# Kernel optimization log

Measured on AMD Instinct MI355X. Metric: run time of the kernel, lower is better.

## Reference

```python
import jax, jax.numpy as jnp
import numpy as np

N = 100000
E = 1600000
NUM_GRAPHS = 64
EPS = 1e-5


def setup_inputs() -> dict:
    key = jax.random.key(0)
    ks = jax.random.split(key, 8)
    x = jax.random.normal(ks[0], (N, 128), dtype=jnp.float32)
    edge_index = jax.random.randint(ks[1], (2, E), 0, N, dtype=jnp.int64)
    batch = jnp.sort(jax.random.randint(ks[2], (N,), 0, NUM_GRAPHS, dtype=jnp.int64))
    W1 = jax.random.normal(ks[3], (128, 128), dtype=jnp.float32) * (1.0 / np.sqrt(128))
    W2 = jax.random.normal(ks[4], (128, 128), dtype=jnp.float32) * (1.0 / np.sqrt(128))
    W3 = jax.random.normal(ks[5], (128, 32), dtype=jnp.float32) * (1.0 / np.sqrt(128))
    return {
        'x': x, 'edge_index': edge_index, 'batch': batch,
        'W1': W1, 'b1': jnp.zeros((128,), jnp.float32),
        'W2': W2, 'b2': jnp.zeros((128,), jnp.float32),
        'W3': W3, 'b3': jnp.zeros((32,), jnp.float32),
        'gamma1': jnp.ones((128,), jnp.float32), 'beta1': jnp.zeros((128,), jnp.float32),
        'gamma2': jnp.ones((128,), jnp.float32), 'beta2': jnp.zeros((128,), jnp.float32),
    }


def _gcn_norm(edge_index, n_nodes):
    # PyG GCNConv default: add self-loops, symmetric normalization.
    loop = jnp.arange(n_nodes, dtype=edge_index.dtype)
    src = jnp.concatenate([edge_index[0], loop])  # [E+N]
    dst = jnp.concatenate([edge_index[1], loop])
    deg = jax.ops.segment_sum(jnp.ones_like(dst, dtype=jnp.float32), dst,
                              num_segments=n_nodes)
    dinv = jnp.where(deg > 0, jax.lax.rsqrt(deg), 0.0)
    norm = dinv[src] * dinv[dst]  # [E+N]
    return src, dst, norm


def _gcn_conv(x, W, b, src, dst, norm, n_nodes):
    h = x @ W                                   # [N, d_out] dense GEMM
    msg = h[src] * norm[:, None]                # gather + scale  [E+N, d_out]
    out = jax.ops.segment_sum(msg, dst, num_segments=n_nodes)  # scatter-add
    return out + b


def _batchnorm(x, gamma, beta):
    # Training-mode BatchNorm1d: batch stats over node dim, biased variance.
    mean = jnp.mean(x, axis=0)
    var = jnp.var(x, axis=0)
    return (x - mean) * jax.lax.rsqrt(var + EPS) * gamma + beta


def reference(x, edge_index, batch, W1, b1, W2, b2, W3, b3,
              gamma1, beta1, gamma2, beta2):
    src, dst, norm = _gcn_norm(edge_index, N)
    h = _gcn_conv(x, W1, b1, src, dst, norm, N)
    h = jax.nn.relu(_batchnorm(h, gamma1, beta1))  # dropout is identity (eval)
    h = _gcn_conv(h, W2, b2, src, dst, norm, N)
    h = jax.nn.relu(_batchnorm(h, gamma2, beta2))
    h = _gcn_conv(h, W3, b3, src, dst, norm, N)
    # global_mean_pool over graph ids
    sums = jax.ops.segment_sum(h, batch, num_segments=NUM_GRAPHS)  # [G, out]
    cnts = jax.ops.segment_sum(jnp.ones((N,), jnp.float32), batch,
                               num_segments=NUM_GRAPHS)
    pooled = sums / jnp.maximum(cnts, 1.0)[:, None]
    return jax.nn.sigmoid(pooled)
```

## Files before the change

### kernel.cpp

```cpp
#include <hip/hip_runtime.h>
#include <math.h>

#define NGRAPH 64
#define EPS_BN 1e-5f
#define BN_BLOCKS 512

typedef unsigned int uint32;
typedef unsigned short ushort16;
typedef __attribute__((ext_vector_type(8))) short short8v;
typedef __attribute__((ext_vector_type(4))) float float4v;

__device__ __forceinline__ float bf2f(uint32 u16) {
    return __uint_as_float(u16 << 16);
}
__device__ __forceinline__ ushort16 f2bf(float f) {
    uint32 u = __float_as_uint(f);
    return (ushort16)((u + 0x7fffu + ((u >> 16) & 1u)) >> 16);
}
__device__ __forceinline__ uint32 pack2(float lo, float hi) {
    return (uint32)f2bf(lo) | ((uint32)f2bf(hi) << 16);
}

__global__ __launch_bounds__(256) void k_cnt(const int* __restrict__ dst, int* cnt, int ne) {
    int i = blockIdx.x * 256 + threadIdx.x;
    if (i < ne) atomicAdd(&cnt[dst[i]], 1);
}

__global__ __launch_bounds__(1024) void k_scan1(const int* __restrict__ cnt,
                                                int* __restrict__ rowstart,
                                                int* __restrict__ blocksum,
                                                float* __restrict__ dinv, int n) {
    __shared__ int sh[1024];
    const int tid = threadIdx.x;
    const int i = blockIdx.x * 1024 + tid;
    int v = (i < n) ? cnt[i] : 0;
    if (i < n) dinv[i] = rsqrtf((float)(v + 1));
    sh[tid] = v;
    __syncthreads();
    for (int off = 1; off < 1024; off <<= 1) {
        int t = (tid >= off) ? sh[tid - off] : 0;
        __syncthreads();
        sh[tid] += t;
        __syncthreads();
    }
    if (i < n) rowstart[i] = sh[tid] - v;
    if (tid == 1023) blocksum[blockIdx.x] = sh[1023];
}

__global__ __launch_bounds__(1024) void k_scan2(int* __restrict__ blocksum, int nb) {
    __shared__ int sh[1024];
    const int tid = threadIdx.x;
    int v = (tid < nb) ? blocksum[tid] : 0;
    sh[tid] = v;
    __syncthreads();
    for (int off = 1; off < 1024; off <<= 1) {
        int t = (tid >= off) ? sh[tid - off] : 0;
        __syncthreads();
        sh[tid] += t;
        __syncthreads();
    }
    if (tid < nb) blocksum[tid] = sh[tid] - v;
}

__global__ __launch_bounds__(256) void k_scan3(int* __restrict__ rowstart,
                                               int* __restrict__ rowcur,
                                               const int* __restrict__ blocksum, int n) {
    int i = blockIdx.x * 256 + threadIdx.x;
    if (i < n) {
        int v = rowstart[i] + blocksum[i >> 10];
        rowstart[i] = v;
        rowcur[i] = v;
    }
}

#define SC_EPB 8
__global__ __launch_bounds__(256) void k_scatter_w(const int* __restrict__ src,
                                                   const int* __restrict__ dst,
                                                   int* __restrict__ rowcur,
                                                   int* __restrict__ esrc,
                                                   int ne, int wsz) {
    const int w = blockIdx.x & 7;
    const int chunk = blockIdx.x >> 3;
    const int wlo = w * wsz;
    const int whi = wlo + wsz;
    int base = chunk * (256 * SC_EPB) + threadIdx.x;
    #pragma unroll
    for (int j = 0; j < SC_EPB; ++j) {
        int i = base + j * 256;
        if (i < ne) {
            int d = dst[i];
            if (d >= wlo && d < whi) {
                int pos = atomicAdd(&rowcur[d], 1);
                esrc[pos] = src[i];
            }
        }
    }
}

__global__ __launch_bounds__(256) void k_wprep(const float* __restrict__ W,
                                               ushort16* __restrict__ Wt,
                                               int rows, int cols) {
    int i = blockIdx.x * 256 + threadIdx.x;
    if (i >= rows * cols) return;
    int c = i / rows, k = i % rows;
    Wt[i] = f2bf(W[k * cols + c]);
}

template<int COLS, bool BN, bool AF32>
__global__ __launch_bounds__(256) void k_gemm_mfma(const void* __restrict__ Av,
                                                   const ushort16* __restrict__ Wt,
                                                   const float* __restrict__ ss,
                                                   ushort16* __restrict__ C, int nrows) {
    constexpr int K = 128;
    constexpr int LDK = K + 8;
    __shared__ ushort16 As[64 * LDK];
    __shared__ ushort16 Bs[COLS * LDK];
    const int tid = threadIdx.x;
    const int row0 = blockIdx.x * 64;

    {
        const uint4* wg = (const uint4*)Wt;
        for (int i = tid; i < COLS * (K / 8); i += 256) {
            int r = i >> 4, c8 = i & 15;
            *(uint4*)&Bs[r * LDK + c8 * 8] = wg[i];
        }
    }
    if constexpr (AF32) {
        const float* A = (const float*)Av;
        for (int i = tid; i < 64 * (K / 4); i += 256) {
            int r = i >> 5, c4 = i & 31;
            float4 a;
            if (row0 + r < nrows) a = *(const float4*)&A[(size_t)(row0 + r) * K + c4 * 4];
            else a = make_float4(0.f, 0.f, 0.f, 0.f);
            if (BN) {
                float4 sc = *(const float4*)&ss[c4 * 4];
                float4 sh = *(const float4*)&ss[128 + c4 * 4];
                a.x = fmaxf(fmaf(a.x, sc.x, sh.x), 0.f);
                a.y = fmaxf(fmaf(a.y, sc.y, sh.y), 0.f);
                a.z = fmaxf(fmaf(a.z, sc.z, sh.z), 0.f);
                a.w = fmaxf(fmaf(a.w, sc.w, sh.w), 0.f);
            }
            ushort4 o;
            o.x = f2bf(a.x); o.y = f2bf(a.y); o.z = f2bf(a.z); o.w = f2bf(a.w);
            *(ushort4*)&As[r * LDK + c4 * 4] = o;
        }
    } else {
        const uint4* Ag = (const uint4*)Av;
        for (int i = tid; i < 64 * (K / 8); i += 256) {
            int r = i >> 4, c8 = i & 15;
            uint4 u;
            if (row0 + r < nrows) u = Ag[(size_t)(row0 + r) * 16 + c8];
            else u = make_uint4(0, 0, 0, 0);
            if (BN) {
                uint32 wv[4] = {u.x, u.y, u.z, u.w};
                #pragma unroll
                for (int t = 0; t < 4; ++t) {
                    int f = c8 * 8 + t * 2;
                    float lo = fmaxf(fmaf(bf2f(wv[t] & 0xffffu), ss[f],     ss[128 + f]),     0.f);
                    float hi = fmaxf(fmaf(bf2f(wv[t] >> 16),     ss[f + 1], ss[128 + f + 1]), 0.f);
                    wv[t] = pack2(lo, hi);
                }
                u.x = wv[0]; u.y = wv[1]; u.z = wv[2]; u.w = wv[3];
            }
            *(uint4*)&As[r * LDK + c8 * 8] = u;
        }
    }
    __syncthreads();

    const int w = tid >> 6;
    const int l = tid & 63;
    const int lr = l & 15;
    const int lg = l >> 4;
    constexpr int CT = COLS / 16;

    float4v acc[CT] = {};
    short8v afrag[4];
    #pragma unroll
    for (int kk = 0; kk < 4; ++kk)
        afrag[kk] = *(const short8v*)&As[(w * 16 + lr) * LDK + kk * 32 + lg * 8];
    #pragma unroll
    for (int kk = 0; kk < 4; ++kk) {
        #pragma unroll
        for (int ct = 0; ct < CT; ++ct) {
            short8v b = *(const short8v*)&Bs[(ct * 16 + lr) * LDK + kk * 32 + lg * 8];
            acc[ct] = __builtin_amdgcn_mfma_f32_16x16x32_bf16(afrag[kk], b, acc[ct], 0, 0, 0);
        }
    }
    #pragma unroll
    for (int ct = 0; ct < CT; ++ct) {
        #pragma unroll
        for (int r = 0; r < 4; ++r) {
            int gr = row0 + w * 16 + lg * 4 + r;
            if (gr < nrows) C[(size_t)gr * COLS + ct * 16 + lr] = f2bf(acc[ct][r]);
        }
    }
}

template<int COLS>
__global__ __launch_bounds__(256) void k_agg_csr(const ushort16* __restrict__ h,
                                                 const int* __restrict__ rowstart,
                                                 const int* __restrict__ cnt,
                                                 const int* __restrict__ esrc,
                                                 const float* __restrict__ dinv,
                                                 uint32* __restrict__ out, int n) {
    constexpr int TPN = COLS / 2;
    const uint32* __restrict__ hu = (const uint32*)h;
    int gt = blockIdx.x * 256 + threadIdx.x;
    int node = gt / TPN;
    if (node >= n) return;
    int lane = gt % TPN;

    float di = dinv[node];
    uint32 p = hu[(size_t)node * TPN + lane];
    float ax = bf2f(p & 0xffffu) * di * di;
    float ay = bf2f(p >> 16) * di * di;

    const int beg = rowstart[node];
    const int end = beg + cnt[node];
    int e = beg;
    for (; e + 4 <= end; e += 4) {
        int s0 = esrc[e], s1 = esrc[e + 1], s2 = esrc[e + 2], s3 = esrc[e + 3];
        float w0 = dinv[s0] * di, w1 = dinv[s1] * di;
        float w2 = dinv[s2] * di, w3 = dinv[s3] * di;
        uint32 p0 = hu[(size_t)s0 * TPN + lane];
        uint32 p1 = hu[(size_t)s1 * TPN + lane];
        uint32 p2 = hu[(size_t)s2 * TPN + lane];
        uint32 p3 = hu[(size_t)s3 * TPN + lane];
        ax = fmaf(bf2f(p0 & 0xffffu), w0, ax); ay = fmaf(bf2f(p0 >> 16), w0, ay);
        ax = fmaf(bf2f(p1 & 0xffffu), w1, ax); ay = fmaf(bf2f(p1 >> 16), w1, ay);
        ax = fmaf(bf2f(p2 & 0xffffu), w2, ax); ay = fmaf(bf2f(p2 >> 16), w2, ay);
        ax = fmaf(bf2f(p3 & 0xffffu), w3, ax); ay = fmaf(bf2f(p3 >> 16), w3, ay);
    }
    for (; e < end; ++e) {
        int s0 = esrc[e];
        float w0 = dinv[s0] * di;
        uint32 p0 = hu[(size_t)s0 * TPN + lane];
        ax = fmaf(bf2f(p0 & 0xffffu), w0, ax);
        ay = fmaf(bf2f(p0 >> 16), w0, ay);
    }
    out[(size_t)node * TPN + lane] = pack2(ax, ay);
}

__global__ __launch_bounds__(256) void k_bn_stats1(const uint32* __restrict__ x,
                                                   float* __restrict__ partials, int n) {
    const int cp = threadIdx.x & 63;
    const int rl = threadIdx.x >> 6;
    float s0 = 0.f, s1 = 0.f, q0 = 0.f, q1 = 0.f;
    for (int r = blockIdx.x * 4 + rl; r < n; r += BN_BLOCKS * 4) {
        uint32 u = x[(size_t)r * 64 + cp];
        float lo = bf2f(u & 0xffffu), hi = bf2f(u >> 16);
        s0 += lo; s1 += hi;
        q0 = fmaf(lo, lo, q0); q1 = fmaf(hi, hi, q1);
    }
    __shared__ float shs[4 * 128];
    __shared__ float shq[4 * 128];
    shs[rl * 128 + 2 * cp] = s0; shs[rl * 128 + 2 * cp + 1] = s1;
    shq[rl * 128 + 2 * cp] = q0; shq[rl * 128 + 2 * cp + 1] = q1;
    __syncthreads();
    int f = threadIdx.x;
    if (f < 128) {
        float s = shs[f] + shs[128 + f] + shs[256 + f] + shs[384 + f];
        float q = shq[f] + shq[128 + f] + shq[256 + f] + shq[384 + f];
        partials[(size_t)blockIdx.x * 256 + f] = s;
        partials[(size_t)blockIdx.x * 256 + 128 + f] = q;
    }
}

__global__ __launch_bounds__(256) void k_bn_stats2(const float* __restrict__ partials,
                                                   float* __restrict__ stats) {
    int j = threadIdx.x;
    float acc = 0.f;
    int r0 = blockIdx.x * (BN_BLOCKS / 8);
    for (int r = 0; r < BN_BLOCKS / 8; ++r)
        acc += partials[(size_t)(r0 + r) * 256 + j];
    atomicAdd(&stats[j], acc);
}

__global__ __launch_bounds__(128) void k_bn_final(const float* __restrict__ stats,
                                                  const float* __restrict__ gamma,
                                                  const float* __restrict__ beta,
                                                  float* __restrict__ ss, int n) {
    int f = threadIdx.x;
    float inv_n = 1.0f / (float)n;
    float mean = stats[f] * inv_n;
    float var = stats[128 + f] * inv_n - mean * mean;
    float scale = gamma[f] * rsqrtf(var + EPS_BN);
    ss[f] = scale;
    ss[128 + f] = beta[f] - mean * scale;
}

#define POOL_SLICE 128
__global__ __launch_bounds__(256) void k_pool2(const uint32* __restrict__ h3,
                                               const int* __restrict__ batch,
                                               float* __restrict__ sums,
                                               float* __restrict__ cnt, int n) {
    const int fp = threadIdx.x & 15;
    const int sub = threadIdx.x >> 4;
    int node0 = blockIdx.x * (16 * POOL_SLICE) + sub * POOL_SLICE;
    if (node0 >= n) return;
    int node1 = min(node0 + POOL_SLICE, n);

    int cur_g = batch[node0];
    float a0 = 0.f, a1 = 0.f, c = 0.f;
    for (int i = node0; i < node1; ++i) {
        int g = batch[i];
        if (g != cur_g) {
            atomicAdd(&sums[cur_g * 32 + 2 * fp], a0);
            atomicAdd(&sums[cur_g * 32 + 2 * fp + 1], a1);
            if (fp == 0) atomicAdd(&cnt[cur_g], c);
            a0 = 0.f; a1 = 0.f; c = 0.f; cur_g = g;
        }
        uint32 u = h3[(size_t)i * 16 + fp];
        a0 += bf2f(u & 0xffffu);
        a1 += bf2f(u >> 16);
        c += 1.f;
    }
    atomicAdd(&sums[cur_g * 32 + 2 * fp], a0);
    atomicAdd(&sums[cur_g * 32 + 2 * fp + 1], a1);
    if (fp == 0) atomicAdd(&cnt[cur_g], c);
}

__global__ __launch_bounds__(256) void k_final(const float* __restrict__ sums,
                                               const float* __restrict__ cnt,
                                               const float* __restrict__ b3,
                                               float* __restrict__ out) {
    int i = blockIdx.x * 256 + threadIdx.x;
    if (i >= NGRAPH * 32) return;
    int g = i >> 5;
    int f = i & 31;
    float c = fmaxf(cnt[g], 1.0f);
    float v = sums[i] / c + b3[f];
    out[i] = 1.0f / (1.0f + expf(-v));
}

extern "C" void kernel_launch(void* const* d_in, const int* in_sizes, int n_in,
                              void* d_out, int out_size, void* d_ws, size_t ws_size,
                              hipStream_t stream) {
    const float* x      = (const float*)d_in[0];
    const int*   eidx   = (const int*)d_in[1];
    const int*   batch  = (const int*)d_in[2];
    const float* W1     = (const float*)d_in[3];
    const float* W2     = (const float*)d_in[5];
    const float* W3     = (const float*)d_in[7];
    const float* b3     = (const float*)d_in[8];
    const float* gamma1 = (const float*)d_in[9];
    const float* beta1  = (const float*)d_in[10];
    const float* gamma2 = (const float*)d_in[11];
    const float* beta2  = (const float*)d_in[12];

    const int N = in_sizes[0] / 128;
    const int E = in_sizes[1] / 2;
    const int* src = eidx;
    const int* dst = eidx + E;

    size_t off = 0;
    auto carve = [&](size_t bytes) {
        char* p = (char*)d_ws + off;
        off += (bytes + 511) & ~(size_t)511;
        return p;
    };
    const size_t NB = (size_t)N * 128 * sizeof(float);
    ushort16* bufA  = (ushort16*)carve(NB / 2);
    uint32* bufB    = (uint32*)carve(NB / 2);
    int*   cnt      = (int*)carve((size_t)N * 4);
    int*   rowstart = (int*)carve((size_t)N * 4);
    int*   rowcur   = (int*)carve((size_t)N * 4);
    float* dinv     = (float*)carve((size_t)N * 4);
    int*   esrc     = (int*)carve((size_t)E * 4);
    ushort16* wt1   = (ushort16*)carve(128 * 128 * 2);
    ushort16* wt2   = (ushort16*)carve(128 * 128 * 2);
    ushort16* wt3   = (ushort16*)carve(32 * 128 * 2);
    float* stats    = (float*)carve(256 * 4);
    float* ss1      = (float*)carve(256 * 4);
    float* ss2      = (float*)carve(256 * 4);
    float* partials = (float*)carve((size_t)BN_BLOCKS * 256 * 4);
    int*   blocksum = (int*)carve(1024 * 4);
    float* psum     = (float*)carve(NGRAPH * 32 * 4);
    float* pcnt     = (float*)carve(NGRAPH * 4);
    (void)ws_size; (void)n_in; (void)out_size;

    const int nblkN   = (N + 255) / 256;
    const int nblkE   = (E + 255) / 256;
    const int nbScan  = (N + 1023) / 1024;
    const int nbGemm  = (N + 63) / 64;
    const int nblkAgg128 = ((size_t)N * 64 + 255) / 256;
    const int nblkAgg32  = ((size_t)N * 16 + 255) / 256;
    const int nblkPool   = (N + 16 * POOL_SLICE - 1) / (16 * POOL_SLICE);
    const int wsz        = (N + 7) / 8;
    const int nbScat     = ((E + 256 * SC_EPB - 1) / (256 * SC_EPB)) * 8;

    k_wprep<<<(128 * 128 + 255) / 256, 256, 0, stream>>>(W1, wt1, 128, 128);
    k_wprep<<<(128 * 128 + 255) / 256, 256, 0, stream>>>(W2, wt2, 128, 128);
    k_wprep<<<(32 * 128 + 255) / 256, 256, 0, stream>>>(W3, wt3, 128, 32);

    hipMemsetAsync(cnt, 0, (size_t)N * 4, stream);
    k_cnt<<<nblkE, 256, 0, stream>>>(dst, cnt, E);
    k_scan1<<<nbScan, 1024, 0, stream>>>(cnt, rowstart, blocksum, dinv, N);
    k_scan2<<<1, 1024, 0, stream>>>(blocksum, nbScan);
    k_scan3<<<nblkN, 256, 0, stream>>>(rowstart, rowcur, blocksum, N);
    k_scatter_w<<<nbScat, 256, 0, stream>>>(src, dst, rowcur, esrc, E, wsz);

    k_gemm_mfma<128, false, true><<<nbGemm, 256, 0, stream>>>(x, wt1, nullptr, bufA, N);
    k_agg_csr<128><<<nblkAgg128, 256, 0, stream>>>(bufA, rowstart, cnt, esrc, dinv, bufB, N);
    k_bn_stats1<<<BN_BLOCKS, 256, 0, stream>>>(bufB, partials, N);
    hipMemsetAsync(stats, 0, 256 * 4, stream);
    k_bn_stats2<<<8, 256, 0, stream>>>(partials, stats);
    k_bn_final<<<1, 128, 0, stream>>>(stats, gamma1, beta1, ss1, N);

    k_gemm_mfma<128, true, false><<<nbGemm, 256, 0, stream>>>(bufB, wt2, ss1, bufA, N);
    k_agg_csr<128><<<nblkAgg128, 256, 0, stream>>>(bufA, rowstart, cnt, esrc, dinv, bufB, N);
    k_bn_stats1<<<BN_BLOCKS, 256, 0, stream>>>(bufB, partials, N);
    hipMemsetAsync(stats, 0, 256 * 4, stream);
    k_bn_stats2<<<8, 256, 0, stream>>>(partials, stats);
    k_bn_final<<<1, 128, 0, stream>>>(stats, gamma2, beta2, ss2, N);

    k_gemm_mfma<32, true, false><<<nbGemm, 256, 0, stream>>>(bufB, wt3, ss2, bufA, N);
    k_agg_csr<32><<<nblkAgg32, 256, 0, stream>>>(bufA, rowstart, cnt, esrc, dinv, bufB, N);

    hipMemsetAsync(psum, 0, NGRAPH * 32 * 4, stream);
    hipMemsetAsync(pcnt, 0, NGRAPH * 4, stream);
    k_pool2<<<nblkPool, 256, 0, stream>>>(bufB, batch, psum, pcnt, N);
    k_final<<<(NGRAPH * 32 + 255) / 256, 256, 0, stream>>>(psum, pcnt, b3, (float*)d_out);
}
```

Measured before the change: 477.0 us.

## Window degree counting, merge weight prep, process two row tiles per GEMM block, unroll gather

The degree-count kernel now uses the same 8-way destination windowing as the scatter kernel, which keeps each block's atomics within a narrower address range. The three weight-prep launches are merged into a single kernel. The GEMM now computes two 64-row tiles per block, reusing the weight tile already staged in shared memory. The CSR aggregation loop is unrolled to 8 edges with all loads issued before the FMAs, to raise memory-level parallelism. The costs are that the count kernel rereads dst 8 times and the GEMM grid is halved.

```diff
diff --git a/kernel.cpp b/kernel.cpp
--- a/kernel.cpp
+++ b/kernel.cpp
@@ -21,9 +21,22 @@
     return (uint32)f2bf(lo) | ((uint32)f2bf(hi) << 16);
 }
 
-__global__ __launch_bounds__(256) void k_cnt(const int* __restrict__ dst, int* cnt, int ne) {
-    int i = blockIdx.x * 256 + threadIdx.x;
-    if (i < ne) atomicAdd(&cnt[dst[i]], 1);
+#define SC_EPB 8
+__global__ __launch_bounds__(256) void k_cnt_w(const int* __restrict__ dst, int* __restrict__ cnt,
+                                               int ne, int wsz) {
+    const int w = blockIdx.x & 7;
+    const int chunk = blockIdx.x >> 3;
+    const int wlo = w * wsz;
+    const int whi = wlo + wsz;
+    int base = chunk * (256 * SC_EPB) + threadIdx.x;
+    #pragma unroll
+    for (int j = 0; j < SC_EPB; ++j) {
+        int i = base + j * 256;
+        if (i < ne) {
+            int d = dst[i];
+            if (d >= wlo && d < whi) atomicAdd(&cnt[d], 1);
+        }
+    }
 }
 
 __global__ __launch_bounds__(1024) void k_scan1(const int* __restrict__ cnt,
@@ -73,7 +86,6 @@
     }
 }
 
-#define SC_EPB 8
 __global__ __launch_bounds__(256) void k_scatter_w(const int* __restrict__ src,
                                                    const int* __restrict__ dst,
                                                    int* __restrict__ rowcur,
@@ -97,13 +109,25 @@
     }
 }
 
-__global__ __launch_bounds__(256) void k_wprep(const float* __restrict__ W,
-                                               ushort16* __restrict__ Wt,
-                                               int rows, int cols) {
+__global__ __launch_bounds__(256) void k_wprep_all(const float* __restrict__ W1,
+                                                   const float* __restrict__ W2,
+                                                   const float* __restrict__ W3,
+                                                   ushort16* __restrict__ wt1,
+                                                   ushort16* __restrict__ wt2,
+                                                   ushort16* __restrict__ wt3) {
     int i = blockIdx.x * 256 + threadIdx.x;
-    if (i >= rows * cols) return;
-    int c = i / rows, k = i % rows;
-    Wt[i] = f2bf(W[k * cols + c]);
+    if (i < 16384) {
+        int c = i >> 7, k = i & 127;
+        wt1[i] = f2bf(W1[k * 128 + c]);
+    } else if (i < 32768) {
+        int j = i - 16384;
+        int c = j >> 7, k = j & 127;
+        wt2[j] = f2bf(W2[k * 128 + c]);
+    } else if (i < 36864) {
+        int j = i - 32768;
+        int c = j >> 7, k = j & 127;
+        wt3[j] = f2bf(W3[k * 32 + c]);
+    }
 }
 
 template<int COLS, bool BN, bool AF32>
@@ -116,7 +140,6 @@
     __shared__ ushort16 As[64 * LDK];
     __shared__ ushort16 Bs[COLS * LDK];
     const int tid = threadIdx.x;
-    const int row0 = blockIdx.x * 64;
 
     {
         const uint4* wg = (const uint4*)Wt;
@@ -125,47 +148,6 @@
             *(uint4*)&Bs[r * LDK + c8 * 8] = wg[i];
         }
     }
-    if constexpr (AF32) {
-        const float* A = (const float*)Av;
-        for (int i = tid; i < 64 * (K / 4); i += 256) {
-            int r = i >> 5, c4 = i & 31;
-            float4 a;
-            if (row0 + r < nrows) a = *(const float4*)&A[(size_t)(row0 + r) * K + c4 * 4];
-            else a = make_float4(0.f, 0.f, 0.f, 0.f);
-            if (BN) {
-                float4 sc = *(const float4*)&ss[c4 * 4];
-                float4 sh = *(const float4*)&ss[128 + c4 * 4];
-                a.x = fmaxf(fmaf(a.x, sc.x, sh.x), 0.f);
-                a.y = fmaxf(fmaf(a.y, sc.y, sh.y), 0.f);
-                a.z = fmaxf(fmaf(a.z, sc.z, sh.z), 0.f);
-                a.w = fmaxf(fmaf(a.w, sc.w, sh.w), 0.f);
-            }
-            ushort4 o;
-            o.x = f2bf(a.x); o.y = f2bf(a.y); o.z = f2bf(a.z); o.w = f2bf(a.w);
-            *(ushort4*)&As[r * LDK + c4 * 4] = o;
-        }
-    } else {
-        const uint4* Ag = (const uint4*)Av;
-        for (int i = tid; i < 64 * (K / 8); i += 256) {
-            int r = i >> 4, c8 = i & 15;
-            uint4 u;
-            if (row0 + r < nrows) u = Ag[(size_t)(row0 + r) * 16 + c8];
-            else u = make_uint4(0, 0, 0, 0);
-            if (BN) {
-                uint32 wv[4] = {u.x, u.y, u.z, u.w};
-                #pragma unroll
-                for (int t = 0; t < 4; ++t) {
-                    int f = c8 * 8 + t * 2;
-                    float lo = fmaxf(fmaf(bf2f(wv[t] & 0xffffu), ss[f],     ss[128 + f]),     0.f);
-                    float hi = fmaxf(fmaf(bf2f(wv[t] >> 16),     ss[f + 1], ss[128 + f + 1]), 0.f);
-                    wv[t] = pack2(lo, hi);
-                }
-                u.x = wv[0]; u.y = wv[1]; u.z = wv[2]; u.w = wv[3];
-            }
-            *(uint4*)&As[r * LDK + c8 * 8] = u;
-        }
-    }
-    __syncthreads();
 
     const int w = tid >> 6;
     const int l = tid & 63;
@@ -173,25 +155,72 @@
     const int lg = l >> 4;
     constexpr int CT = COLS / 16;
 
-    float4v acc[CT] = {};
-    short8v afrag[4];
     #pragma unroll
-    for (int kk = 0; kk < 4; ++kk)
-        afrag[kk] = *(const short8v*)&As[(w * 16 + lr) * LDK + kk * 32 + lg * 8];
-    #pragma unroll
-    for (int kk = 0; kk < 4; ++kk) {
+    for (int half = 0; half < 2; ++half) {
+        const int row0 = blockIdx.x * 128 + half * 64;
+        if (half) __syncthreads();
+        if constexpr (AF32) {
+            const float* A = (const float*)Av;
+            for (int i = tid; i < 64 * (K / 4); i += 256) {
+                int r = i >> 5, c4 = i & 31;
+                float4 a;
+                if (row0 + r < nrows) a = *(const float4*)&A[(size_t)(row0 + r) * K + c4 * 4];
+                else a = make_float4(0.f, 0.f, 0.f, 0.f);
+                if (BN) {
+                    float4 sc = *(const float4*)&ss[c4 * 4];
+                    float4 sh = *(const float4*)&ss[128 + c4 * 4];
+                    a.x = fmaxf(fmaf(a.x, sc.x, sh.x), 0.f);
+                    a.y = fmaxf(fmaf(a.y, sc.y, sh.y), 0.f);
+                    a.z = fmaxf(fmaf(a.z, sc.z, sh.z), 0.f);
+                    a.w = fmaxf(fmaf(a.w, sc.w, sh.w), 0.f);
+                }
+                ushort4 o;
+                o.x = f2bf(a.x); o.y = f2bf(a.y); o.z = f2bf(a.z); o.w = f2bf(a.w);
+                *(ushort4*)&As[r * LDK + c4 * 4] = o;
+            }
+        } else {
+            const uint4* Ag = (const uint4*)Av;
+            for (int i = tid; i < 64 * (K / 8); i += 256) {
+                int r = i >> 4, c8 = i & 15;
+                uint4 u;
+                if (row0 + r < nrows) u = Ag[(size_t)(row0 + r) * 16 + c8];
+                else u = make_uint4(0, 0, 0, 0);
+                if (BN) {
+                    uint32 wv[4] = {u.x, u.y, u.z, u.w};
+                    #pragma unroll
+                    for (int t = 0; t < 4; ++t) {
+                        int f = c8 * 8 + t * 2;
+                        float lo = fmaxf(fmaf(bf2f(wv[t] & 0xffffu), ss[f],     ss[128 + f]),     0.f);
+                        float hi = fmaxf(fmaf(bf2f(wv[t] >> 16),     ss[f + 1], ss[128 + f + 1]), 0.f);
+                        wv[t] = pack2(lo, hi);
+                    }
+                    u.x = wv[0]; u.y = wv[1]; u.z = wv[2]; u.w = wv[3];
+                }
+                *(uint4*)&As[r * LDK + c8 * 8] = u;
+            }
+        }
+        __syncthreads();
+
+        float4v acc[CT] = {};
+        short8v afrag[4];
+        #pragma unroll
+        for (int kk = 0; kk < 4; ++kk)
+            afrag[kk] = *(const short8v*)&As[(w * 16 + lr) * LDK + kk * 32 + lg * 8];
+        #pragma unroll
+        for (int kk = 0; kk < 4; ++kk) {
+            #pragma unroll
+            for (int ct = 0; ct < CT; ++ct) {
+                short8v b = *(const short8v*)&Bs[(ct * 16 + lr) * LDK + kk * 32 + lg * 8];
+                acc[ct] = __builtin_amdgcn_mfma_f32_16x16x32_bf16(afrag[kk], b, acc[ct], 0, 0, 0);
+            }
+        }
         #pragma unroll
         for (int ct = 0; ct < CT; ++ct) {
-            short8v b = *(const short8v*)&Bs[(ct * 16 + lr) * LDK + kk * 32 + lg * 8];
-            acc[ct] = __builtin_amdgcn_mfma_f32_16x16x32_bf16(afrag[kk], b, acc[ct], 0, 0, 0);
-        }
-    }
-    #pragma unroll
-    for (int ct = 0; ct < CT; ++ct) {
-        #pragma unroll
-        for (int r = 0; r < 4; ++r) {
-            int gr = row0 + w * 16 + lg * 4 + r;
-            if (gr < nrows) C[(size_t)gr * COLS + ct * 16 + lr] = f2bf(acc[ct][r]);
+            #pragma unroll
+            for (int r = 0; r < 4; ++r) {
+                int gr = row0 + w * 16 + lg * 4 + r;
+                if (gr < nrows) C[(size_t)gr * COLS + ct * 16 + lr] = f2bf(acc[ct][r]);
+            }
         }
     }
 }
@@ -218,18 +247,19 @@
     const int beg = rowstart[node];
     const int end = beg + cnt[node];
     int e = beg;
-    for (; e + 4 <= end; e += 4) {
-        int s0 = esrc[e], s1 = esrc[e + 1], s2 = esrc[e + 2], s3 = esrc[e + 3];
-        float w0 = dinv[s0] * di, w1 = dinv[s1] * di;
-        float w2 = dinv[s2] * di, w3 = dinv[s3] * di;
-        uint32 p0 = hu[(size_t)s0 * TPN + lane];
-        uint32 p1 = hu[(size_t)s1 * TPN + lane];
-        uint32 p2 = hu[(size_t)s2 * TPN + lane];
-        uint32 p3 = hu[(size_t)s3 * TPN + lane];
-        ax = fmaf(bf2f(p0 & 0xffffu), w0, ax); ay = fmaf(bf2f(p0 >> 16), w0, ay);
-        ax = fmaf(bf2f(p1 & 0xffffu), w1, ax); ay = fmaf(bf2f(p1 >> 16), w1, ay);
-        ax = fmaf(bf2f(p2 & 0xffffu), w2, ax); ay = fmaf(bf2f(p2 >> 16), w2, ay);
-        ax = fmaf(bf2f(p3 & 0xffffu), w3, ax); ay = fmaf(bf2f(p3 >> 16), w3, ay);
+    for (; e + 8 <= end; e += 8) {
+        int s[8]; uint32 pp[8]; float w[8];
+        #pragma unroll
+        for (int j = 0; j < 8; ++j) s[j] = esrc[e + j];
+        #pragma unroll
+        for (int j = 0; j < 8; ++j) pp[j] = hu[(size_t)s[j] * TPN + lane];
+        #pragma unroll
+        for (int j = 0; j < 8; ++j) w[j] = dinv[s[j]] * di;
+        #pragma unroll
+        for (int j = 0; j < 8; ++j) {
+            ax = fmaf(bf2f(pp[j] & 0xffffu), w[j], ax);
+            ay = fmaf(bf2f(pp[j] >> 16), w[j], ay);
+        }
     }
     for (; e < end; ++e) {
         int s0 = esrc[e];
@@ -380,21 +410,18 @@
     (void)ws_size; (void)n_in; (void)out_size;
 
     const int nblkN   = (N + 255) / 256;
-    const int nblkE   = (E + 255) / 256;
     const int nbScan  = (N + 1023) / 1024;
-    const int nbGemm  = (N + 63) / 64;
+    const int nbGemm  = (N + 127) / 128;
     const int nblkAgg128 = ((size_t)N * 64 + 255) / 256;
     const int nblkAgg32  = ((size_t)N * 16 + 255) / 256;
     const int nblkPool   = (N + 16 * POOL_SLICE - 1) / (16 * POOL_SLICE);
     const int wsz        = (N + 7) / 8;
     const int nbScat     = ((E + 256 * SC_EPB - 1) / (256 * SC_EPB)) * 8;
 
-    k_wprep<<<(128 * 128 + 255) / 256, 256, 0, stream>>>(W1, wt1, 128, 128);
-    k_wprep<<<(128 * 128 + 255) / 256, 256, 0, stream>>>(W2, wt2, 128, 128);
-    k_wprep<<<(32 * 128 + 255) / 256, 256, 0, stream>>>(W3, wt3, 128, 32);
+    k_wprep_all<<<(36864 + 255) / 256, 256, 0, stream>>>(W1, W2, W3, wt1, wt2, wt3);
 
     hipMemsetAsync(cnt, 0, (size_t)N * 4, stream);
-    k_cnt<<<nblkE, 256, 0, stream>>>(dst, cnt, E);
+    k_cnt_w<<<nbScat, 256, 0, stream>>>(dst, cnt, E, wsz);
     k_scan1<<<nbScan, 1024, 0, stream>>>(cnt, rowstart, blocksum, dinv, N);
     k_scan2<<<1, 1024, 0, stream>>>(blocksum, nbScan);
     k_scan3<<<nblkN, 256, 0, stream>>>(rowstart, rowcur, blocksum, N);
```

Result: no change. 481.8 us (+1.0%).
